# Performance work log

Hardware: AMD Instinct MI355X
Metric: run time of the kernel (lower is better)

The kernel has to match this reference:

```python
import jax, jax.numpy as jnp
import numpy as np

STEP = 0.1          # step_size
MAX_STEPS = 50      # max_steps
MAX_CURV = 100.0    # max_curvature
DX = 1.0            # grid_spacing
B, H, W, D = 2, 96, 96, 96


def _gradient(f):
    # central differences with replicate (edge) padding; f: (B,H,W,D)
    fp = jnp.pad(f, ((0, 0), (1, 1), (1, 1), (1, 1)), mode='edge')
    gx = (fp[:, 2:, 1:-1, 1:-1] - fp[:, :-2, 1:-1, 1:-1]) / (2 * DX)
    gy = (fp[:, 1:-1, 2:, 1:-1] - fp[:, 1:-1, :-2, 1:-1]) / (2 * DX)
    gz = (fp[:, 1:-1, 1:-1, 2:] - fp[:, 1:-1, 1:-1, :-2]) / (2 * DX)
    return jnp.stack([gx, gy, gz], axis=-1)  # (B,H,W,D,3)


def _christoffel(Phi):
    # Gamma^i_jk = d_ij g_k + d_ik g_j - d_jk g_i with g = grad(Phi)
    g = _gradient(Phi)                       # (B,H,W,D,3)
    I = jnp.eye(3, dtype=Phi.dtype)
    return (I[:, :, None] * g[..., None, None, :]
            + I[:, None, :] * g[..., None, :, None]
            - I[None, :, :] * g[..., :, None, None])  # (B,H,W,D,3,3,3)


def _accel(pos, vel, Gamma, dims_f, dims_i):
    # nearest-cell lookup of Gamma at normalized positions, then a^i = -G^i_jk v^j v^k
    idx = jnp.clip((pos * dims_f).astype(jnp.int32), 0, dims_i)  # (B,3)
    b = jnp.arange(pos.shape[0])
    G = Gamma[b, idx[:, 0], idx[:, 1], idx[:, 2]]  # (B,3,3,3)
    a = -jnp.einsum('bijk,bj,bk->bi', G, vel, vel)
    return jnp.clip(a, -MAX_CURV, MAX_CURV)


def _rk4_step(pos, vel, Gamma, dims_f, dims_i):
    h = STEP
    k1v = vel
    k1a = _accel(pos, vel, Gamma, dims_f, dims_i)
    k2v = vel + 0.5 * h * k1a
    k2a = _accel(pos + 0.5 * h * k1v, k2v, Gamma, dims_f, dims_i)
    k3v = vel + 0.5 * h * k2a
    k3a = _accel(pos + 0.5 * h * k2v, k3v, Gamma, dims_f, dims_i)
    k4v = vel + h * k3a
    k4a = _accel(pos + h * k3v, k4v, Gamma, dims_f, dims_i)
    pos_new = pos + (h / 6.0) * (k1v + 2 * k2v + 2 * k3v + k4v)
    vel_new = vel + (h / 6.0) * (k1a + 2 * k2a + 2 * k3a + k4a)
    return pos_new, vel_new


def setup_inputs() -> dict:
    key = jax.random.key(0)
    k1, k2, k3 = jax.random.split(key, 3)
    start_pos = jax.random.uniform(k1, (B, 3), dtype=jnp.float32)
    start_vel = jax.random.normal(k2, (B, 3), dtype=jnp.float32)
    Phi = jax.random.normal(k3, (B, H, W, D), dtype=jnp.float32)
    return {"start_pos": start_pos, "start_vel": start_vel, "Phi": Phi}


def reference(start_pos, start_vel, Phi):
    _, h, w, d = Phi.shape
    dims_f = jnp.array([h - 1, w - 1, d - 1], dtype=Phi.dtype)
    dims_i = jnp.array([h - 1, w - 1, d - 1], dtype=jnp.int32)
    Gamma = _christoffel(Phi)  # precomputed once, as in the original

    def step(carry, _):
        pos, vel = carry
        pos, vel = _rk4_step(pos, vel, Gamma, dims_f, dims_i)
        return (pos, vel), (pos, vel)

    _, (ps, vs) = jax.lax.scan(step, (start_pos, start_vel), None, length=MAX_STEPS - 1)
    positions = jnp.concatenate([start_pos[:, None, :], jnp.moveaxis(ps, 0, 1)], axis=1)
    velocities = jnp.concatenate([start_vel[:, None, :], jnp.moveaxis(vs, 0, 1)], axis=1)
    return positions, velocities  # each (B, MAX_STEPS, 3)
```

## Files before the change

### kernel.cpp

```cpp
#include <hip/hip_runtime.h>

#pragma clang fp contract(off)

namespace {

constexpr int HD    = 96;
constexpr int STRX  = HD * HD;
constexpr int VOL   = HD * HD * HD;
constexpr int NSTEPS = 50;
constexpr int DIMI  = HD - 1;
constexpr float DIMF = 95.0f;
constexpr float MAXC = 100.0f;
constexpr unsigned TAG = 0x5A5A0000u;

struct V3 { float x, y, z; };

__device__ __forceinline__ int clampi(int v) {
    return v < 0 ? 0 : (v > DIMI ? DIMI : v);
}

__device__ __forceinline__ int xcc_id() {
    unsigned v;
    asm volatile("s_getreg_b32 %0, hwreg(HW_REG_XCC_ID)" : "=s"(v));
    return (int)(v & 0xFu);
}

__device__ __forceinline__ void warm_slice(const float* __restrict__ base,
                                           int slice, int nslices,
                                           int tid, int nthr) {
    const float4* p4 = (const float4*)base;
    int n4  = VOL / 4;
    int per = (n4 + nslices - 1) / nslices;
    int lo  = slice * per;
    int hi  = lo + per; if (hi > n4) hi = n4;
    float acc = 0.f;
    for (int i = lo + tid; i < hi; i += nthr) {
        float4 v = p4[i];
        acc += v.x + v.y + v.z + v.w;
    }
    asm volatile("" :: "v"(acc));
}

__device__ __forceinline__ void load_nb(const float* __restrict__ base,
                                        const V3 p, float nb[6]) {
    int x = clampi((int)(p.x * DIMF));
    int y = clampi((int)(p.y * DIMF));
    int z = clampi((int)(p.z * DIMF));
    int xp = x < DIMI ? x + 1 : DIMI, xm = x > 0 ? x - 1 : 0;
    int yp = y < DIMI ? y + 1 : DIMI, ym = y > 0 ? y - 1 : 0;
    int zp = z < DIMI ? z + 1 : DIMI, zm = z > 0 ? z - 1 : 0;
    int rowx = x * STRX;
    nb[0] = base[xp * STRX + y * HD + z];
    nb[1] = base[xm * STRX + y * HD + z];
    nb[2] = base[rowx + yp * HD + z];
    nb[3] = base[rowx + ym * HD + z];
    nb[4] = base[rowx + y * HD + zp];
    nb[5] = base[rowx + y * HD + zm];
}

__device__ __forceinline__ V3 accel_from(const float nb[6], const V3 v) {
    float gx = (nb[0] - nb[1]) * 0.5f;
    float gy = (nb[2] - nb[3]) * 0.5f;
    float gz = (nb[4] - nb[5]) * 0.5f;
    float gv = gx * v.x + gy * v.y + gz * v.z;
    float vv = v.x * v.x + v.y * v.y + v.z * v.z;
    V3 a;
    a.x = -(2.0f * v.x * gv - gx * vv);
    a.y = -(2.0f * v.y * gv - gy * vv);
    a.z = -(2.0f * v.z * gv - gz * vv);
    a.x = fminf(fmaxf(a.x, -MAXC), MAXC);
    a.y = fminf(fmaxf(a.y, -MAXC), MAXC);
    a.z = fminf(fmaxf(a.z, -MAXC), MAXC);
    return a;
}

__device__ __forceinline__ V3 axpy(const V3 a, float s, const V3 b) {
    V3 r; r.x = a.x + s * b.x; r.y = a.y + s * b.y; r.z = a.z + s * b.z;
    return r;
}

}

__global__ void __launch_bounds__(256)
geodesic_kernel(const float* __restrict__ sp, const float* __restrict__ sv,
                const float* __restrict__ Phi, float* __restrict__ out,
                int B, unsigned* __restrict__ ws) {
    int xcc = xcc_id();

    if (blockIdx.x < (unsigned)B) {
        int b = blockIdx.x;
        const float* __restrict__ base = Phi + (long)b * VOL;

        if (threadIdx.x == 0) {
            __hip_atomic_store(&ws[b], TAG | (unsigned)xcc,
                               __ATOMIC_RELAXED, __HIP_MEMORY_SCOPE_AGENT);
        }
        if (threadIdx.x >= 64) {
            warm_slice(base, 0, 16, threadIdx.x - 64, 192);
            return;
        }
        if (threadIdx.x != 0) return;

        __builtin_amdgcn_s_setprio(1);

        const float H   = 0.1f;
        const float H05 = 0.5f * H;
        const float H6  = (float)(0.1 / 6.0);

        float* __restrict__ opos = out;
        float* __restrict__ ovel = out + (long)B * NSTEPS * 3;

        V3 pos = { sp[b * 3 + 0], sp[b * 3 + 1], sp[b * 3 + 2] };
        V3 vel = { sv[b * 3 + 0], sv[b * 3 + 1], sv[b * 3 + 2] };

        long o0 = (long)b * NSTEPS * 3;
        opos[o0 + 0] = pos.x; opos[o0 + 1] = pos.y; opos[o0 + 2] = pos.z;
        ovel[o0 + 0] = vel.x; ovel[o0 + 1] = vel.y; ovel[o0 + 2] = vel.z;

        for (int t = 1; t < NSTEPS; ++t) {
            V3 p1 = pos;
            V3 p2 = axpy(pos, H05, vel);
            float nb1[6], nb2[6];
            load_nb(base, p1, nb1);
            load_nb(base, p2, nb2);

            V3 k1a = accel_from(nb1, vel);
            V3 k2v = axpy(vel, H05, k1a);
            V3 k2a = accel_from(nb2, k2v);
            V3 k3v = axpy(vel, H05, k2a);

            V3 p3 = axpy(pos, H05, k2v);
            V3 p4 = axpy(pos, H, k3v);
            float nb3[6], nb4[6];
            load_nb(base, p3, nb3);
            load_nb(base, p4, nb4);

            V3 k3a = accel_from(nb3, k3v);
            V3 k4v = axpy(vel, H, k3a);
            V3 k4a = accel_from(nb4, k4v);

            V3 sv_;
            sv_.x = vel.x + 2.0f * k2v.x + 2.0f * k3v.x + k4v.x;
            sv_.y = vel.y + 2.0f * k2v.y + 2.0f * k3v.y + k4v.y;
            sv_.z = vel.z + 2.0f * k2v.z + 2.0f * k3v.z + k4v.z;
            V3 sa;
            sa.x = k1a.x + 2.0f * k2a.x + 2.0f * k3a.x + k4a.x;
            sa.y = k1a.y + 2.0f * k2a.y + 2.0f * k3a.y + k4a.y;
            sa.z = k1a.z + 2.0f * k2a.z + 2.0f * k3a.z + k4a.z;
            pos = axpy(pos, H6, sv_);
            vel = axpy(vel, H6, sa);

            long ot = (long)b * NSTEPS * 3 + (long)t * 3;
            opos[ot + 0] = pos.x; opos[ot + 1] = pos.y; opos[ot + 2] = pos.z;
            ovel[ot + 0] = vel.x; ovel[ot + 1] = vel.y; ovel[ot + 2] = vel.z;
        }
        return;
    }

    __shared__ int sh[2];
    if (threadIdx.x == 0) {
        int t0 = -1, t1 = -1;
        for (int it = 0; it < 8192; ++it) {
            unsigned a = __hip_atomic_load(&ws[0], __ATOMIC_RELAXED,
                                           __HIP_MEMORY_SCOPE_AGENT);
            unsigned c = __hip_atomic_load(&ws[1], __ATOMIC_RELAXED,
                                           __HIP_MEMORY_SCOPE_AGENT);
            if ((a & 0xFFFF0000u) == TAG) t0 = (int)(a & 0xFu);
            if ((c & 0xFFFF0000u) == TAG) t1 = (int)(c & 0xFu);
            if (t0 >= 0 && t1 >= 0) break;
        }
        sh[0] = t0; sh[1] = t1;
    }
    __syncthreads();
    int t0 = sh[0], t1 = sh[1];

    int batch = -1;
    if (xcc == t0 && xcc == t1) batch = (int)(blockIdx.x & 1);
    else if (xcc == t0) batch = 0;
    else if (xcc == t1) batch = 1;
    if (batch < 0) return;

    int slice = 1 + (int)((blockIdx.x >> 3) % 15);
    warm_slice(Phi + (long)batch * VOL, slice, 16, threadIdx.x, 256);
}

extern "C" void kernel_launch(void* const* d_in, const int* in_sizes, int n_in,
                              void* d_out, int out_size, void* d_ws, size_t ws_size,
                              hipStream_t stream) {
    const float* sp  = (const float*)d_in[0];
    const float* sv  = (const float*)d_in[1];
    const float* phi = (const float*)d_in[2];
    float* out = (float*)d_out;
    unsigned* ws = (unsigned*)d_ws;
    int B = in_sizes[0] / 3;

    geodesic_kernel<<<dim3(B + 126), dim3(256), 0, stream>>>(sp, sv, phi, out, B, ws);
}
```

Baseline: 117.2 us.

## Use atomic work-stealing of L2 warm slices per wave and batch all neighbor loads

Replaces the static 16-slice cache-warming split with per-wave dynamic slice claiming through an atomic counter in the workspace, so helper waves on the same XCC as each trajectory thread share warming of the Phi volume in finer 32-slice units. The neighbor addresses for each RK4 stage pair are computed first and all twelve loads are issued together before use, to expose more memory-level parallelism. Helper blocks now poll per wave without the __syncthreads step, and launch bounds request one block per SIMD slot. The counter relies on the workspace starting at a poison value (0xAAAAAAAA), so it is harness-dependent and may skip warming entirely if that assumption fails.

After: 117.6 us. No clear change (+0.3%).

```diff
diff --git a/kernel.cpp b/kernel.cpp
--- a/kernel.cpp
+++ b/kernel.cpp
@@ -8,12 +8,15 @@
 constexpr int STRX  = HD * HD;
 constexpr int VOL   = HD * HD * HD;
 constexpr int NSTEPS = 50;
-constexpr int DIMI  = HD - 1;
+constexpr int DIMI  = 95;
 constexpr float DIMF = 95.0f;
 constexpr float MAXC = 100.0f;
 constexpr unsigned TAG = 0x5A5A0000u;
+constexpr unsigned POISON = 0xAAAAAAAAu;
+constexpr int NSLICE = 32;
 
 struct V3 { float x, y, z; };
+struct Nb6 { const float *p0, *p1, *p2, *p3, *p4, *p5; };
 
 __device__ __forceinline__ int clampi(int v) {
     return v < 0 ? 0 : (v > DIMI ? DIMI : v);
@@ -25,43 +28,29 @@
     return (int)(v & 0xFu);
 }
 
-__device__ __forceinline__ void warm_slice(const float* __restrict__ base,
-                                           int slice, int nslices,
-                                           int tid, int nthr) {
-    const float4* p4 = (const float4*)base;
-    int n4  = VOL / 4;
-    int per = (n4 + nslices - 1) / nslices;
-    int lo  = slice * per;
-    int hi  = lo + per; if (hi > n4) hi = n4;
-    float acc = 0.f;
-    for (int i = lo + tid; i < hi; i += nthr) {
-        float4 v = p4[i];
-        acc += v.x + v.y + v.z + v.w;
-    }
-    asm volatile("" :: "v"(acc));
-}
-
-__device__ __forceinline__ void load_nb(const float* __restrict__ base,
-                                        const V3 p, float nb[6]) {
+__device__ __forceinline__ Nb6 nb_addr(const float* __restrict__ base, V3 p) {
     int x = clampi((int)(p.x * DIMF));
     int y = clampi((int)(p.y * DIMF));
     int z = clampi((int)(p.z * DIMF));
     int xp = x < DIMI ? x + 1 : DIMI, xm = x > 0 ? x - 1 : 0;
     int yp = y < DIMI ? y + 1 : DIMI, ym = y > 0 ? y - 1 : 0;
     int zp = z < DIMI ? z + 1 : DIMI, zm = z > 0 ? z - 1 : 0;
-    int rowx = x * STRX;
-    nb[0] = base[xp * STRX + y * HD + z];
-    nb[1] = base[xm * STRX + y * HD + z];
-    nb[2] = base[rowx + yp * HD + z];
-    nb[3] = base[rowx + ym * HD + z];
-    nb[4] = base[rowx + y * HD + zp];
-    nb[5] = base[rowx + y * HD + zm];
-}
-
-__device__ __forceinline__ V3 accel_from(const float nb[6], const V3 v) {
-    float gx = (nb[0] - nb[1]) * 0.5f;
-    float gy = (nb[2] - nb[3]) * 0.5f;
-    float gz = (nb[4] - nb[5]) * 0.5f;
+    int rowx = x * STRX, coly = y * HD;
+    Nb6 r;
+    r.p0 = base + (xp * STRX + coly + z);
+    r.p1 = base + (xm * STRX + coly + z);
+    r.p2 = base + (rowx + yp * HD + z);
+    r.p3 = base + (rowx + ym * HD + z);
+    r.p4 = base + (rowx + coly + zp);
+    r.p5 = base + (rowx + coly + zm);
+    return r;
+}
+
+__device__ __forceinline__ V3 accel6(float n0, float n1, float n2, float n3,
+                                     float n4, float n5, V3 v) {
+    float gx = (n0 - n1) * 0.5f;
+    float gy = (n2 - n3) * 0.5f;
+    float gz = (n4 - n5) * 0.5f;
     float gv = gx * v.x + gy * v.y + gz * v.z;
     float vv = v.x * v.x + v.y * v.y + v.z * v.z;
     V3 a;
@@ -74,18 +63,41 @@
     return a;
 }
 
-__device__ __forceinline__ V3 axpy(const V3 a, float s, const V3 b) {
+__device__ __forceinline__ V3 axpy(V3 a, float s, V3 b) {
     V3 r; r.x = a.x + s * b.x; r.y = a.y + s * b.y; r.z = a.z + s * b.z;
     return r;
 }
 
-}
-
-__global__ void __launch_bounds__(256)
+__device__ __forceinline__ void warm_wave(const float* __restrict__ base,
+                                          unsigned* __restrict__ ctr, int lane) {
+    const float4* p4 = (const float4*)base;
+    const int per = (VOL / 4) / NSLICE;
+    float acc = 0.f;
+    for (;;) {
+        unsigned old = 0;
+        if (lane == 0)
+            old = __hip_atomic_fetch_add(ctr, 1u, __ATOMIC_RELAXED,
+                                         __HIP_MEMORY_SCOPE_AGENT);
+        old = __shfl(old, 0);
+        unsigned s = old - POISON;
+        if (s >= (unsigned)NSLICE) break;
+        int lo = (int)s * per;
+        for (int i = lo + lane; i < lo + per; i += 64) {
+            float4 v = p4[i];
+            acc += v.x + v.y + v.z + v.w;
+        }
+    }
+    asm volatile("" :: "v"(acc));
+}
+
+}
+
+__global__ void __launch_bounds__(256, 1)
 geodesic_kernel(const float* __restrict__ sp, const float* __restrict__ sv,
                 const float* __restrict__ Phi, float* __restrict__ out,
                 int B, unsigned* __restrict__ ws) {
     int xcc = xcc_id();
+    int lane = threadIdx.x & 63;
 
     if (blockIdx.x < (unsigned)B) {
         int b = blockIdx.x;
@@ -96,7 +108,7 @@
                                __ATOMIC_RELAXED, __HIP_MEMORY_SCOPE_AGENT);
         }
         if (threadIdx.x >= 64) {
-            warm_slice(base, 0, 16, threadIdx.x - 64, 192);
+            warm_wave(base, &ws[2 + b], lane);
             return;
         }
         if (threadIdx.x != 0) return;
@@ -120,24 +132,30 @@
         for (int t = 1; t < NSTEPS; ++t) {
             V3 p1 = pos;
             V3 p2 = axpy(pos, H05, vel);
-            float nb1[6], nb2[6];
-            load_nb(base, p1, nb1);
-            load_nb(base, p2, nb2);
-
-            V3 k1a = accel_from(nb1, vel);
+            Nb6 A = nb_addr(base, p1);
+            Nb6 Bq = nb_addr(base, p2);
+            float a0 = *A.p0,  a1 = *A.p1,  a2 = *A.p2,
+                  a3 = *A.p3,  a4 = *A.p4,  a5 = *A.p5;
+            float b0 = *Bq.p0, b1 = *Bq.p1, b2 = *Bq.p2,
+                  b3 = *Bq.p3, b4 = *Bq.p4, b5 = *Bq.p5;
+
+            V3 k1a = accel6(a0, a1, a2, a3, a4, a5, vel);
             V3 k2v = axpy(vel, H05, k1a);
-            V3 k2a = accel_from(nb2, k2v);
+            V3 k2a = accel6(b0, b1, b2, b3, b4, b5, k2v);
             V3 k3v = axpy(vel, H05, k2a);
 
             V3 p3 = axpy(pos, H05, k2v);
             V3 p4 = axpy(pos, H, k3v);
-            float nb3[6], nb4[6];
-            load_nb(base, p3, nb3);
-            load_nb(base, p4, nb4);
-
-            V3 k3a = accel_from(nb3, k3v);
+            Nb6 C = nb_addr(base, p3);
+            Nb6 D = nb_addr(base, p4);
+            float c0 = *C.p0, c1 = *C.p1, c2 = *C.p2,
+                  c3 = *C.p3, c4 = *C.p4, c5 = *C.p5;
+            float d0 = *D.p0, d1 = *D.p1, d2 = *D.p2,
+                  d3 = *D.p3, d4 = *D.p4, d5 = *D.p5;
+
+            V3 k3a = accel6(c0, c1, c2, c3, c4, c5, k3v);
             V3 k4v = axpy(vel, H, k3a);
-            V3 k4a = accel_from(nb4, k4v);
+            V3 k4a = accel6(d0, d1, d2, d3, d4, d5, k4v);
 
             V3 sv_;
             sv_.x = vel.x + 2.0f * k2v.x + 2.0f * k3v.x + k4v.x;
@@ -157,31 +175,28 @@
         return;
     }
 
-    __shared__ int sh[2];
-    if (threadIdx.x == 0) {
-        int t0 = -1, t1 = -1;
-        for (int it = 0; it < 8192; ++it) {
-            unsigned a = __hip_atomic_load(&ws[0], __ATOMIC_RELAXED,
-                                           __HIP_MEMORY_SCOPE_AGENT);
-            unsigned c = __hip_atomic_load(&ws[1], __ATOMIC_RELAXED,
-                                           __HIP_MEMORY_SCOPE_AGENT);
-            if ((a & 0xFFFF0000u) == TAG) t0 = (int)(a & 0xFu);
-            if ((c & 0xFFFF0000u) == TAG) t1 = (int)(c & 0xFu);
-            if (t0 >= 0 && t1 >= 0) break;
-        }
-        sh[0] = t0; sh[1] = t1;
+    unsigned w0 = 0, w1 = 0;
+    if (lane == 0) {
+        for (int it = 0; it < 65536; ++it) {
+            w0 = __hip_atomic_load(&ws[0], __ATOMIC_RELAXED,
+                                   __HIP_MEMORY_SCOPE_AGENT);
+            w1 = __hip_atomic_load(&ws[1], __ATOMIC_RELAXED,
+                                   __HIP_MEMORY_SCOPE_AGENT);
+            if ((w0 & 0xFFFF0000u) == TAG && (w1 & 0xFFFF0000u) == TAG) break;
+        }
     }
-    __syncthreads();
-    int t0 = sh[0], t1 = sh[1];
+    w0 = __shfl(w0, 0);
+    w1 = __shfl(w1, 0);
+    int t0 = ((w0 & 0xFFFF0000u) == TAG) ? (int)(w0 & 0xFu) : -1;
+    int t1 = ((w1 & 0xFFFF0000u) == TAG) ? (int)(w1 & 0xFu) : -1;
 
     int batch = -1;
-    if (xcc == t0 && xcc == t1) batch = (int)(blockIdx.x & 1);
-    else if (xcc == t0) batch = 0;
-    else if (xcc == t1) batch = 1;
+    if (xcc == t0 && xcc == t1)      batch = (int)(blockIdx.x & 1);
+    else if (xcc == t0)              batch = 0;
+    else if (xcc == t1)              batch = 1;
     if (batch < 0) return;
 
-    int slice = 1 + (int)((blockIdx.x >> 3) % 15);
-    warm_slice(Phi + (long)batch * VOL, slice, 16, threadIdx.x, 256);
+    warm_wave(Phi + (long)batch * VOL, &ws[2 + batch], lane);
 }
 
 extern "C" void kernel_launch(void* const* d_in, const int* in_sizes, int n_in,
```
